# Kernel tuning notes

Hardware: AMD Instinct MI355X
Metric: run time of the kernel (lower is better)

## Reference

```python
import jax, jax.numpy as jnp
import numpy as np

NODES_PER_GRAPH = 57
NUM_BRANCHES = 80
NUM_GRAPHS = 4096
IN_CH = 4
HID = 128
NUM_LAYERS = 5
BN_EPS = 1e-5


def setup_inputs() -> dict:
    key = jax.random.key(0)
    ks = jax.random.split(key, 24)
    N = NUM_GRAPHS * NODES_PER_GRAPH
    E = NUM_GRAPHS * NUM_BRANCHES * 2  # bidirectional branches per graph
    x = jax.random.normal(ks[0], (N, IN_CH), dtype=jnp.float32)
    # within-graph random edges, offset per graph block
    ep = jax.random.randint(ks[1], (2, E), 0, NODES_PER_GRAPH, dtype=jnp.int32)
    off = jnp.repeat(jnp.arange(NUM_GRAPHS, dtype=jnp.int32) * NODES_PER_GRAPH,
                     NUM_BRANCHES * 2)
    edge_index = ep + off[None, :]
    i = np.arange(NUM_BRANCHES)
    branch_u = jnp.asarray(i % NODES_PER_GRAPH, dtype=jnp.int32)
    branch_v = jnp.asarray((i * 7 + 3) % NODES_PER_GRAPH, dtype=jnp.int32)
    s = 0.05
    return {
        "x": x, "edge_index": edge_index,
        "branch_u": branch_u, "branch_v": branch_v,
        "Wp": jax.random.normal(ks[2], (IN_CH, HID)) * s,
        "bp": jnp.zeros((HID,), jnp.float32),
        "conv_W": jax.random.normal(ks[3], (NUM_LAYERS, HID, HID)) * s,
        "conv_b": jnp.zeros((NUM_LAYERS, HID), jnp.float32),
        "bn_gamma": jnp.ones((NUM_LAYERS, HID), jnp.float32),
        "bn_beta": jnp.zeros((NUM_LAYERS, HID), jnp.float32),
        "bn_mean": jax.random.normal(ks[4], (NUM_LAYERS, HID)) * 0.1,
        "bn_var": jax.random.uniform(ks[5], (NUM_LAYERS, HID)) + 0.5,
        "phys_W1": jax.random.normal(ks[6], (HID, 16)) * s,
        "phys_b1": jnp.zeros((16,), jnp.float32),
        "phys_W2": jax.random.normal(ks[7], (16, 1)) * s,
        "phys_b2": jnp.zeros((1,), jnp.float32),
        "mlp_W1": jax.random.normal(ks[8], (2 * HID + 1, HID)) * s,
        "mlp_b1": jnp.zeros((HID,), jnp.float32),
        "mlp_W2": jax.random.normal(ks[9], (HID, 1)) * s,
        "mlp_b2": jnp.zeros((1,), jnp.float32),
    }


def _gcn_conv(x, edge_index, W, b, num_nodes):
    # PyG GCNConv: add self-loops, symmetric deg^{-1/2} normalization,
    # message = norm * (x @ W)[src], scatter-add into dst, then + bias.
    h = x @ W
    loop = jnp.arange(num_nodes, dtype=edge_index.dtype)
    src = jnp.concatenate([edge_index[0], loop])
    dst = jnp.concatenate([edge_index[1], loop])
    deg = jax.ops.segment_sum(jnp.ones_like(dst, dtype=h.dtype), dst,
                              num_segments=num_nodes)  # >= 1 (self-loop)
    dinv = jax.lax.rsqrt(deg)
    norm = dinv[src] * dinv[dst]  # [E+N]
    out = jax.ops.segment_sum(h[src] * norm[:, None], dst,
                              num_segments=num_nodes)
    return out + b


def _forward(x, edge_index, branch_u, branch_v, Wp, bp, conv_W, conv_b,
             bn_gamma, bn_beta, bn_mean, bn_var, phys_W1, phys_b1, phys_W2,
             phys_b2, mlp_W1, mlp_b1, mlp_W2, mlp_b2):
    N = x.shape[0]
    num_graphs = N // NODES_PER_GRAPH
    h = x @ Wp + bp
    for l in range(NUM_LAYERS):
        res = h
        h = _gcn_conv(h, edge_index, conv_W[l], conv_b[l], N)
        # BatchNorm1d in eval mode (running stats); dropout is identity in eval
        h = (h - bn_mean[l]) * jax.lax.rsqrt(bn_var[l] + BN_EPS) * bn_gamma[l] + bn_beta[l]
        h = jax.nn.relu(h)
        h = h + res
    theta = jax.nn.relu(h @ phys_W1 + phys_b1) @ phys_W2 + phys_b2  # [N,1]
    offsets = (jnp.arange(num_graphs, dtype=jnp.int32) * NODES_PER_GRAPH)
    u_idx = (branch_u[None, :] + offsets[:, None]).reshape(-1)
    v_idx = (branch_v[None, :] + offsets[:, None]).reshape(-1)
    edge_feat = jnp.concatenate([h[u_idx], h[v_idx]], axis=-1)  # [G*80, 2H]
    delta_theta = theta[u_idx] - theta[v_idx]                   # [G*80, 1]
    comb = jnp.concatenate([edge_feat, delta_theta], axis=-1)
    return jax.nn.relu(comb @ mlp_W1 + mlp_b1) @ mlp_W2 + mlp_b2


def reference(x, edge_index, branch_u, branch_v, Wp, bp, conv_W, conv_b,
              bn_gamma, bn_beta, bn_mean, bn_var, phys_W1, phys_b1, phys_W2,
              phys_b2, mlp_W1, mlp_b1, mlp_W2, mlp_b2):
    return _forward(x, edge_index, branch_u, branch_v, Wp, bp, conv_W, conv_b,
                    bn_gamma, bn_beta, bn_mean, bn_var, phys_W1, phys_b1,
                    phys_W2, phys_b2, mlp_W1, mlp_b1, mlp_W2, mlp_b2)
```

## Files before the change

### kernel.cpp

```cpp
#include <hip/hip_runtime.h>

#define NPG 57
#define NEPG 160
#define NB 80
#define HID 128
#define NG 4096
#define NL 5

typedef __attribute__((ext_vector_type(8))) short bf16x8;
typedef __attribute__((ext_vector_type(4))) float f32x4;
typedef unsigned int u32;

__device__ __forceinline__ short f2bf(float f) {
    u32 u = __builtin_bit_cast(u32, f);
    u += 0x7fff + ((u >> 16) & 1);
    return (short)(u >> 16);
}
__device__ __forceinline__ float bf2f(short s) {
    u32 u = ((u32)(unsigned short)s) << 16;
    return __builtin_bit_cast(float, u);
}
__device__ __forceinline__ u32 packhl(float v) {
    short hi = f2bf(v);
    short lo = f2bf(v - bf2f(hi));
    return (((u32)(unsigned short)hi) << 16) | (u32)(unsigned short)lo;
}
__device__ __forceinline__ float unpackf(u32 u) {
    return bf2f((short)(u >> 16)) + bf2f((short)(u & 0xFFFFu));
}

__device__ __forceinline__ void unpack_frag(uint4 a, uint4 b, bf16x8& fh, bf16x8& fl) {
    uint4 h, l;
    h.x = (a.y & 0xFFFF0000u) | (a.x >> 16);
    h.y = (a.w & 0xFFFF0000u) | (a.z >> 16);
    h.z = (b.y & 0xFFFF0000u) | (b.x >> 16);
    h.w = (b.w & 0xFFFF0000u) | (b.z >> 16);
    l.x = (a.y << 16) | (a.x & 0xFFFFu);
    l.y = (a.w << 16) | (a.z & 0xFFFFu);
    l.z = (b.y << 16) | (b.x & 0xFFFFu);
    l.w = (b.w << 16) | (b.z & 0xFFFFu);
    fh = __builtin_bit_cast(bf16x8, h);
    fl = __builtin_bit_cast(bf16x8, l);
}

__device__ __forceinline__ void frag_pk(const u32* rowp, int k0, int sw,
                                        bf16x8& fh, bf16x8& fl) {
    uint4 a = *(const uint4*)((const char*)rowp + ((k0 * 4) ^ sw));
    uint4 b = *(const uint4*)((const char*)rowp + (((k0 + 4) * 4) ^ sw));
    unpack_frag(a, b, fh, fl);
}

template<int NCT>
__device__ __forceinline__ void mm_ks(f32x4* acc, const bf16x8& fh, const bf16x8& fl,
                                      const short* __restrict__ whi,
                                      const short* __restrict__ wlo,
                                      int ln15, int kb, int ks, int ctbase) {
#pragma unroll
    for (int j = 0; j < NCT; ++j) {
        int ct = ctbase + j;
        bf16x8 bhi = *(const bf16x8*)(whi + (16 * ct + ln15) * HID + kb + 32 * ks);
        bf16x8 blo = *(const bf16x8*)(wlo + (16 * ct + ln15) * HID + kb + 32 * ks);
        f32x4 a = acc[j];
        a = __builtin_amdgcn_mfma_f32_16x16x32_bf16(fh, bhi, a, 0, 0, 0);
        a = __builtin_amdgcn_mfma_f32_16x16x32_bf16(fh, blo, a, 0, 0, 0);
        a = __builtin_amdgcn_mfma_f32_16x16x32_bf16(fl, bhi, a, 0, 0, 0);
        acc[j] = a;
    }
}

__global__ void prep(const float* __restrict__ convW, const float* __restrict__ mlpW1,
                     const float* __restrict__ physW1, const float* __restrict__ convb,
                     const float* __restrict__ bn_gamma, const float* __restrict__ bn_beta,
                     const float* __restrict__ bn_mean, const float* __restrict__ bn_var,
                     short* __restrict__ wb, float* __restrict__ fsc, float* __restrict__ fsh) {
    int id = blockIdx.x * 256 + threadIdx.x;
    if (id < 114688) {
        int mat = id >> 14, rem = id & 16383, n = rem >> 7, k = rem & 127;
        float w;
        if (mat < 5)       w = convW[mat * 16384 + k * 128 + n];
        else if (mat == 5) w = mlpW1[k * 128 + n];
        else               w = mlpW1[(128 + k) * 128 + n];
        short hi = f2bf(w);
        short lo = f2bf(w - bf2f(hi));
        wb[mat * 32768 + n * 128 + k] = hi;
        wb[mat * 32768 + 16384 + n * 128 + k] = lo;
    } else if (id < 116736) {
        int p = id - 114688, n = p >> 7, k = p & 127;
        float w = physW1[k * 16 + n];
        short hi = f2bf(w);
        short lo = f2bf(w - bf2f(hi));
        wb[229376 + p] = hi;
        wb[231424 + p] = lo;
    } else if (id < 117376) {
        int p = id - 116736;
        float sc = bn_gamma[p] * rsqrtf(bn_var[p] + 1e-5f);
        float sh = fmaf(convb[p] - bn_mean[p], sc, bn_beta[p]);
        fsc[p] = sc;
        fsh[p] = sh;
    }
}

__global__ __launch_bounds__(1024, 4) void pinn_fused(
    const float* __restrict__ x, const int* __restrict__ edge_index,
    const int* __restrict__ branch_u, const int* __restrict__ branch_v,
    const float* __restrict__ Wp, const float* __restrict__ bp,
    const float* __restrict__ physb1, const float* __restrict__ physW2,
    const float* __restrict__ physb2,
    const float* __restrict__ mlpW1, const float* __restrict__ mlpb1,
    const float* __restrict__ mlpW2, const float* __restrict__ mlpb2,
    const short* __restrict__ wb, const float* __restrict__ fsc,
    const float* __restrict__ fsh, float* __restrict__ out) {
    __shared__ u32  hTu[128][64];
    __shared__ u32  pool[64 * 128];
    __shared__ short Ahi[64 * 64];
    __shared__ short Alo[64 * 64];
    __shared__ float dinv[64];
    __shared__ int   deg[64];
    __shared__ short esrc[NEPG], edst[NEPG];
    __shared__ float theta[64];
    __shared__ float red[NB];
    __shared__ int   bu[NB], bv[NB];

    const int g = blockIdx.x;
    const int tid = threadIdx.x;
    const int lane = tid & 63;
    const int wv = tid >> 6;
    const int ln15 = lane & 15;
    const int hi4 = lane >> 4;
    const int kb = hi4 << 3;
    const int R0 = 16 * (wv & 3);
    const int ct0 = 2 * (wv >> 2);

    {
        int r = lane;
        float4 xv = make_float4(0.f, 0.f, 0.f, 0.f);
        if (r < NPG) xv = ((const float4*)x)[g * NPG + r];
        for (int c = 8 * wv; c < 8 * wv + 8; ++c) {
            float h0 = 0.f;
            if (r < NPG)
                h0 = fmaf(xv.x, Wp[c], fmaf(xv.y, Wp[HID + c],
                     fmaf(xv.z, Wp[2 * HID + c], fmaf(xv.w, Wp[3 * HID + c], bp[c]))));
            *(u32*)((char*)&hTu[c][0] + ((r * 4) ^ ((c & 7) << 4))) = packhl(h0);
        }
    }
    if (tid < 64) deg[tid] = (tid < NPG) ? 1 : 0;
    if (tid < NB) { bu[tid] = branch_u[tid]; bv[tid] = branch_v[tid]; red[tid] = 0.f; }
    {
        float* Af = (float*)pool;
        for (int i = tid; i < 4096; i += 1024) Af[i] = 0.f;
    }
    __syncthreads();

    if (tid < NEPG) {
        int gs = edge_index[g * NEPG + tid];
        int gd = edge_index[NG * NEPG + g * NEPG + tid];
        esrc[tid] = (short)(gs - g * NPG);
        edst[tid] = (short)(gd - g * NPG);
        atomicAdd(&deg[edst[tid]], 1);
    }
    __syncthreads();
    if (tid < 64) dinv[tid] = (tid < NPG) ? rsqrtf((float)deg[tid]) : 0.f;
    __syncthreads();
    {
        float* Af = (float*)pool;
        if (tid < NEPG) {
            int s = esrc[tid], d = edst[tid];
            atomicAdd(&Af[d * 64 + s], dinv[s] * dinv[d]);
        }
        if (tid < NPG) atomicAdd(&Af[tid * 64 + tid], dinv[tid] * dinv[tid]);
    }
    __syncthreads();
    {
        const float* Af = (const float*)pool;
        for (int i = tid; i < 4096; i += 1024) {
            float a = Af[i];
            short hi = f2bf(a);
            Ahi[i] = hi;
            Alo[i] = f2bf(a - bf2f(hi));
        }
    }
    __syncthreads();

    bf16x8 afh[2], afl[2];
#pragma unroll
    for (int ks2 = 0; ks2 < 2; ++ks2) {
        int off = (R0 + ln15) * 64 + 32 * ks2 + kb;
        afh[ks2] = *(const bf16x8*)&Ahi[off];
        afl[ks2] = *(const bf16x8*)&Alo[off];
    }

    u32* mpk = pool;
    for (int l = 0; l < NL; ++l) {
        f32x4 acc[2];
        acc[0] = (f32x4){0.f, 0.f, 0.f, 0.f};
        acc[1] = (f32x4){0.f, 0.f, 0.f, 0.f};
#pragma unroll
        for (int ks2 = 0; ks2 < 2; ++ks2) {
#pragma unroll
            for (int j = 0; j < 2; ++j) {
                int c = 16 * (ct0 + j) + ln15;
                bf16x8 hh, hl;
                frag_pk(&hTu[c][0], 32 * ks2 + kb, (c & 7) << 4, hh, hl);
                f32x4 a = acc[j];
                a = __builtin_amdgcn_mfma_f32_16x16x32_bf16(afh[ks2], hh, a, 0, 0, 0);
                a = __builtin_amdgcn_mfma_f32_16x16x32_bf16(afh[ks2], hl, a, 0, 0, 0);
                a = __builtin_amdgcn_mfma_f32_16x16x32_bf16(afl[ks2], hh, a, 0, 0, 0);
                acc[j] = a;
            }
        }
#pragma unroll
        for (int j = 0; j < 2; ++j) {
#pragma unroll
            for (int q = 0; q < 4; ++q) {
                int rr = R0 + 4 * hi4 + q;
                int cc = 16 * (ct0 + j) + ln15;
                *(u32*)((char*)&mpk[rr * 128] + ((cc * 4) ^ ((rr & 7) << 4))) =
                    packhl(acc[j][q]);
            }
        }
        __syncthreads();

        f32x4 z2[2];
        z2[0] = (f32x4){0.f, 0.f, 0.f, 0.f};
        z2[1] = (f32x4){0.f, 0.f, 0.f, 0.f};
        const short* whi = wb + 2 * l * 16384;
        const short* wlo = wb + (2 * l + 1) * 16384;
#pragma unroll
        for (int ks = 0; ks < 4; ++ks) {
            bf16x8 mh, ml;
            int rr = R0 + ln15;
            frag_pk(&mpk[rr * 128], 32 * ks + kb, (rr & 7) << 4, mh, ml);
            mm_ks<2>(z2, mh, ml, whi, wlo, ln15, kb, ks, ct0);
        }
        if (l == NL - 1) __syncthreads();

        const float* sc = fsc + l * HID;
        const float* sh = fsh + l * HID;
#pragma unroll
        for (int j = 0; j < 2; ++j) {
            int cc = 16 * (ct0 + j) + ln15;
            float scv = sc[cc], shv = sh[cc];
#pragma unroll
            for (int q = 0; q < 4; ++q) {
                int rr = R0 + 4 * hi4 + q;
                u32* hp = (u32*)((char*)&hTu[cc][0] + ((rr * 4) ^ ((cc & 7) << 4)));
                float hold = unpackf(*hp);
                float hnew = fmaxf(fmaf(z2[j][q], scv, shv), 0.f) + hold;
                if (l == NL - 1)
                    *(u32*)((char*)&pool[rr * 128] + ((cc * 4) ^ ((rr & 7) << 4))) =
                        packhl(hnew);
                else
                    *hp = packhl(hnew);
            }
        }
        __syncthreads();
    }

    if (wv < 4) {
        f32x4 t4 = (f32x4){0.f, 0.f, 0.f, 0.f};
        int r = 16 * wv + ln15;
#pragma unroll
        for (int ks = 0; ks < 4; ++ks) {
            bf16x8 fh, fl;
            frag_pk(&pool[r * 128], 32 * ks + kb, (r & 7) << 4, fh, fl);
            bf16x8 bh = *(const bf16x8*)(wb + 229376 + ln15 * HID + 32 * ks + kb);
            bf16x8 bl = *(const bf16x8*)(wb + 231424 + ln15 * HID + 32 * ks + kb);
            t4 = __builtin_amdgcn_mfma_f32_16x16x32_bf16(fh, bh, t4, 0, 0, 0);
            t4 = __builtin_amdgcn_mfma_f32_16x16x32_bf16(fh, bl, t4, 0, 0, 0);
            t4 = __builtin_amdgcn_mfma_f32_16x16x32_bf16(fl, bh, t4, 0, 0, 0);
        }
        float b1 = physb1[ln15], w2 = physW2[ln15], b2 = physb2[0];
#pragma unroll
        for (int q = 0; q < 4; ++q) {
            float val = fmaxf(t4[q] + b1, 0.f) * w2;
#pragma unroll
            for (int o = 1; o < 16; o <<= 1) val += __shfl_xor(val, o, 16);
            int rq = 16 * wv + 4 * hi4 + q;
            if (ln15 == 0 && rq < NPG) theta[rq] = val + b2;
        }
    }
    __syncthreads();

    for (int task = wv; task < 10; task += 16) {
        int t = task >> 1;
        int cb = (task & 1) * 4;
        int b = 16 * t + ln15;
        int ru = bu[b], rv = bv[b];
        f32x4 acc4[4];
#pragma unroll
        for (int j = 0; j < 4; ++j) acc4[j] = (f32x4){0.f, 0.f, 0.f, 0.f};
#pragma unroll
        for (int ks = 0; ks < 4; ++ks) {
            bf16x8 fh, fl;
            frag_pk(&pool[ru * 128], 32 * ks + kb, (ru & 7) << 4, fh, fl);
            mm_ks<4>(acc4, fh, fl, wb + 10 * 16384, wb + 11 * 16384, ln15, kb, ks, cb);
            frag_pk(&pool[rv * 128], 32 * ks + kb, (rv & 7) << 4, fh, fl);
            mm_ks<4>(acc4, fh, fl, wb + 12 * 16384, wb + 13 * 16384, ln15, kb, ks, cb);
        }
        float dth[4];
#pragma unroll
        for (int q = 0; q < 4; ++q) {
            int bb = 16 * t + 4 * hi4 + q;
            dth[q] = theta[bu[bb]] - theta[bv[bb]];
        }
        float sums[4] = {0.f, 0.f, 0.f, 0.f};
#pragma unroll
        for (int j = 0; j < 4; ++j) {
            int ch = 16 * (cb + j) + ln15;
            float w256 = mlpW1[256 * HID + ch];
            float b1 = mlpb1[ch];
            float w2 = mlpW2[ch];
#pragma unroll
            for (int q = 0; q < 4; ++q)
                sums[q] += fmaxf(fmaf(dth[q], w256, acc4[j][q] + b1), 0.f) * w2;
        }
#pragma unroll
        for (int q = 0; q < 4; ++q) {
#pragma unroll
            for (int o = 1; o < 16; o <<= 1) sums[q] += __shfl_xor(sums[q], o, 16);
            if (ln15 == 0) atomicAdd(&red[16 * t + 4 * hi4 + q], sums[q]);
        }
    }
    __syncthreads();
    if (tid < NB) out[g * NB + tid] = red[tid] + mlpb2[0];
}

extern "C" void kernel_launch(void* const* d_in, const int* in_sizes, int n_in,
                              void* d_out, int out_size, void* d_ws, size_t ws_size,
                              hipStream_t stream) {
    const float* x          = (const float*)d_in[0];
    const int*   edge_index = (const int*)d_in[1];
    const int*   branch_u   = (const int*)d_in[2];
    const int*   branch_v   = (const int*)d_in[3];
    const float* Wp         = (const float*)d_in[4];
    const float* bp         = (const float*)d_in[5];
    const float* convW      = (const float*)d_in[6];
    const float* convb      = (const float*)d_in[7];
    const float* bn_gamma   = (const float*)d_in[8];
    const float* bn_beta    = (const float*)d_in[9];
    const float* bn_mean    = (const float*)d_in[10];
    const float* bn_var     = (const float*)d_in[11];
    const float* physW1     = (const float*)d_in[12];
    const float* physb1     = (const float*)d_in[13];
    const float* physW2     = (const float*)d_in[14];
    const float* physb2     = (const float*)d_in[15];
    const float* mlpW1      = (const float*)d_in[16];
    const float* mlpb1      = (const float*)d_in[17];
    const float* mlpW2      = (const float*)d_in[18];
    const float* mlpb2      = (const float*)d_in[19];
    float* out = (float*)d_out;

    short* wb = (short*)d_ws;
    float* fsc = (float*)((char*)d_ws + 466944);
    float* fsh = fsc + 640;

    prep<<<459, 256, 0, stream>>>(convW, mlpW1, physW1, convb,
                                  bn_gamma, bn_beta, bn_mean, bn_var, wb, fsc, fsh);
    pinn_fused<<<NG, 1024, 0, stream>>>(
        x, edge_index, branch_u, branch_v, Wp, bp,
        physb1, physW2, physb2, mlpW1, mlpb1, mlpW2, mlpb2,
        wb, fsc, fsh, out);
}
```

Before: 1.221 ms.

## Switch split-precision MFMA from bf16 to fp16 with separate hi/lo planes, 512 threads

Replaces the bf16 hi/lo packed-u32 storage with separate fp16 hi and lo shared-memory planes and uses fp16 MFMA. This removes the per-fragment unpack bit manipulation and the pack/unpack work. The block shrinks from 1024 to 512 threads, so each wave now computes four column tiles instead of two. fp16 has a narrower exponent range than bf16, so the split may lose accuracy for very large or very small values, and fewer waves per block may reduce latency hiding.

```diff
diff --git a/kernel.cpp b/kernel.cpp
--- a/kernel.cpp
+++ b/kernel.cpp
@@ -7,72 +7,22 @@
 #define NG 4096
 #define NL 5
 
-typedef __attribute__((ext_vector_type(8))) short bf16x8;
+typedef __attribute__((ext_vector_type(8))) _Float16 f16x8;
+typedef __attribute__((ext_vector_type(4))) _Float16 f16x4;
 typedef __attribute__((ext_vector_type(4))) float f32x4;
-typedef unsigned int u32;
-
-__device__ __forceinline__ short f2bf(float f) {
-    u32 u = __builtin_bit_cast(u32, f);
-    u += 0x7fff + ((u >> 16) & 1);
-    return (short)(u >> 16);
-}
-__device__ __forceinline__ float bf2f(short s) {
-    u32 u = ((u32)(unsigned short)s) << 16;
-    return __builtin_bit_cast(float, u);
-}
-__device__ __forceinline__ u32 packhl(float v) {
-    short hi = f2bf(v);
-    short lo = f2bf(v - bf2f(hi));
-    return (((u32)(unsigned short)hi) << 16) | (u32)(unsigned short)lo;
-}
-__device__ __forceinline__ float unpackf(u32 u) {
-    return bf2f((short)(u >> 16)) + bf2f((short)(u & 0xFFFFu));
-}
-
-__device__ __forceinline__ void unpack_frag(uint4 a, uint4 b, bf16x8& fh, bf16x8& fl) {
-    uint4 h, l;
-    h.x = (a.y & 0xFFFF0000u) | (a.x >> 16);
-    h.y = (a.w & 0xFFFF0000u) | (a.z >> 16);
-    h.z = (b.y & 0xFFFF0000u) | (b.x >> 16);
-    h.w = (b.w & 0xFFFF0000u) | (b.z >> 16);
-    l.x = (a.y << 16) | (a.x & 0xFFFFu);
-    l.y = (a.w << 16) | (a.z & 0xFFFFu);
-    l.z = (b.y << 16) | (b.x & 0xFFFFu);
-    l.w = (b.w << 16) | (b.z & 0xFFFFu);
-    fh = __builtin_bit_cast(bf16x8, h);
-    fl = __builtin_bit_cast(bf16x8, l);
-}
-
-__device__ __forceinline__ void frag_pk(const u32* rowp, int k0, int sw,
-                                        bf16x8& fh, bf16x8& fl) {
-    uint4 a = *(const uint4*)((const char*)rowp + ((k0 * 4) ^ sw));
-    uint4 b = *(const uint4*)((const char*)rowp + (((k0 + 4) * 4) ^ sw));
-    unpack_frag(a, b, fh, fl);
-}
-
-template<int NCT>
-__device__ __forceinline__ void mm_ks(f32x4* acc, const bf16x8& fh, const bf16x8& fl,
-                                      const short* __restrict__ whi,
-                                      const short* __restrict__ wlo,
-                                      int ln15, int kb, int ks, int ctbase) {
-#pragma unroll
-    for (int j = 0; j < NCT; ++j) {
-        int ct = ctbase + j;
-        bf16x8 bhi = *(const bf16x8*)(whi + (16 * ct + ln15) * HID + kb + 32 * ks);
-        bf16x8 blo = *(const bf16x8*)(wlo + (16 * ct + ln15) * HID + kb + 32 * ks);
-        f32x4 a = acc[j];
-        a = __builtin_amdgcn_mfma_f32_16x16x32_bf16(fh, bhi, a, 0, 0, 0);
-        a = __builtin_amdgcn_mfma_f32_16x16x32_bf16(fh, blo, a, 0, 0, 0);
-        a = __builtin_amdgcn_mfma_f32_16x16x32_bf16(fl, bhi, a, 0, 0, 0);
-        acc[j] = a;
-    }
+
+#define MFMA16(A, B, C) __builtin_amdgcn_mfma_f32_16x16x32_f16(A, B, C, 0, 0, 0)
+
+__device__ __forceinline__ f16x8 ldf8(const _Float16* base, int byteoff) {
+    return *(const f16x8*)((const char*)base + byteoff);
 }
 
 __global__ void prep(const float* __restrict__ convW, const float* __restrict__ mlpW1,
                      const float* __restrict__ physW1, const float* __restrict__ convb,
                      const float* __restrict__ bn_gamma, const float* __restrict__ bn_beta,
                      const float* __restrict__ bn_mean, const float* __restrict__ bn_var,
-                     short* __restrict__ wb, float* __restrict__ fsc, float* __restrict__ fsh) {
+                     _Float16* __restrict__ wb, float* __restrict__ fsc,
+                     float* __restrict__ fsh) {
     int id = blockIdx.x * 256 + threadIdx.x;
     if (id < 114688) {
         int mat = id >> 14, rem = id & 16383, n = rem >> 7, k = rem & 127;
@@ -80,27 +30,24 @@
         if (mat < 5)       w = convW[mat * 16384 + k * 128 + n];
         else if (mat == 5) w = mlpW1[k * 128 + n];
         else               w = mlpW1[(128 + k) * 128 + n];
-        short hi = f2bf(w);
-        short lo = f2bf(w - bf2f(hi));
+        _Float16 hi = (_Float16)w;
         wb[mat * 32768 + n * 128 + k] = hi;
-        wb[mat * 32768 + 16384 + n * 128 + k] = lo;
+        wb[mat * 32768 + 16384 + n * 128 + k] = (_Float16)(w - (float)hi);
     } else if (id < 116736) {
         int p = id - 114688, n = p >> 7, k = p & 127;
         float w = physW1[k * 16 + n];
-        short hi = f2bf(w);
-        short lo = f2bf(w - bf2f(hi));
+        _Float16 hi = (_Float16)w;
         wb[229376 + p] = hi;
-        wb[231424 + p] = lo;
+        wb[231424 + p] = (_Float16)(w - (float)hi);
     } else if (id < 117376) {
         int p = id - 116736;
         float sc = bn_gamma[p] * rsqrtf(bn_var[p] + 1e-5f);
-        float sh = fmaf(convb[p] - bn_mean[p], sc, bn_beta[p]);
         fsc[p] = sc;
-        fsh[p] = sh;
+        fsh[p] = fmaf(convb[p] - bn_mean[p], sc, bn_beta[p]);
     }
 }
 
-__global__ __launch_bounds__(1024, 4) void pinn_fused(
+__global__ __launch_bounds__(512, 2) void pinn_fused(
     const float* __restrict__ x, const int* __restrict__ edge_index,
     const int* __restrict__ branch_u, const int* __restrict__ branch_v,
     const float* __restrict__ Wp, const float* __restrict__ bp,
@@ -108,12 +55,12 @@
     const float* __restrict__ physb2,
     const float* __restrict__ mlpW1, const float* __restrict__ mlpb1,
     const float* __restrict__ mlpW2, const float* __restrict__ mlpb2,
-    const short* __restrict__ wb, const float* __restrict__ fsc,
+    const _Float16* __restrict__ wb, const float* __restrict__ fsc,
     const float* __restrict__ fsh, float* __restrict__ out) {
-    __shared__ u32  hTu[128][64];
-    __shared__ u32  pool[64 * 128];
-    __shared__ short Ahi[64 * 64];
-    __shared__ short Alo[64 * 64];
+    __shared__ _Float16 hTh[128 * 64];
+    __shared__ _Float16 hTl[128 * 64];
+    __shared__ _Float16 mh[64 * 128];
+    __shared__ _Float16 ml[64 * 128];
     __shared__ float dinv[64];
     __shared__ int   deg[64];
     __shared__ short esrc[NEPG], edst[NEPG];
@@ -127,28 +74,32 @@
     const int wv = tid >> 6;
     const int ln15 = lane & 15;
     const int hi4 = lane >> 4;
-    const int kb = hi4 << 3;
     const int R0 = 16 * (wv & 3);
-    const int ct0 = 2 * (wv >> 2);
+    const int ct0 = 4 * (wv >> 2);
+
+    float* Af = (float*)mh;
+    _Float16* Ah = ml;
+    _Float16* Al = ml + 4096;
 
     {
-        int r = lane;
-        float4 xv = make_float4(0.f, 0.f, 0.f, 0.f);
-        if (r < NPG) xv = ((const float4*)x)[g * NPG + r];
-        for (int c = 8 * wv; c < 8 * wv + 8; ++c) {
+        int c = tid & 127;
+        int sw = (c & 7) << 4;
+        float w0 = Wp[c], w1 = Wp[HID + c], w2 = Wp[2 * HID + c], w3 = Wp[3 * HID + c];
+        float bb = bp[c];
+        for (int r = tid >> 7; r < 64; r += 4) {
             float h0 = 0.f;
-            if (r < NPG)
-                h0 = fmaf(xv.x, Wp[c], fmaf(xv.y, Wp[HID + c],
-                     fmaf(xv.z, Wp[2 * HID + c], fmaf(xv.w, Wp[3 * HID + c], bp[c]))));
-            *(u32*)((char*)&hTu[c][0] + ((r * 4) ^ ((c & 7) << 4))) = packhl(h0);
-        }
-    }
+            if (r < NPG) {
+                float4 xv = ((const float4*)x)[g * NPG + r];
+                h0 = fmaf(xv.x, w0, fmaf(xv.y, w1, fmaf(xv.z, w2, fmaf(xv.w, w3, bb))));
+            }
+            _Float16 hh = (_Float16)h0;
+            *(_Float16*)((char*)(hTh + c * 64) + ((r * 2) ^ sw)) = hh;
+            *(_Float16*)((char*)(hTl + c * 64) + ((r * 2) ^ sw)) = (_Float16)(h0 - (float)hh);
+        }
+    }
+    for (int i = tid; i < 4096; i += 512) Af[i] = 0.f;
     if (tid < 64) deg[tid] = (tid < NPG) ? 1 : 0;
     if (tid < NB) { bu[tid] = branch_u[tid]; bv[tid] = branch_v[tid]; red[tid] = 0.f; }
-    {
-        float* Af = (float*)pool;
-        for (int i = tid; i < 4096; i += 1024) Af[i] = 0.f;
-    }
     __syncthreads();
 
     if (tid < NEPG) {
@@ -161,113 +112,152 @@
     __syncthreads();
     if (tid < 64) dinv[tid] = (tid < NPG) ? rsqrtf((float)deg[tid]) : 0.f;
     __syncthreads();
+    if (tid < NEPG) {
+        int s = esrc[tid], d = edst[tid];
+        atomicAdd(&Af[d * 64 + s], dinv[s] * dinv[d]);
+    }
+    if (tid < NPG) atomicAdd(&Af[tid * 64 + tid], dinv[tid] * dinv[tid]);
+    __syncthreads();
+    for (int i = tid; i < 4096; i += 512) {
+        int r = i >> 6, s = i & 63;
+        float v = Af[i];
+        _Float16 hi = (_Float16)v;
+        int byteoff = (s * 2) ^ ((r & 7) << 4);
+        *(_Float16*)((char*)(Ah + r * 64) + byteoff) = hi;
+        *(_Float16*)((char*)(Al + r * 64) + byteoff) = (_Float16)(v - (float)hi);
+    }
+    __syncthreads();
+
+    f16x8 Ahf[2], Alf[2];
     {
-        float* Af = (float*)pool;
-        if (tid < NEPG) {
-            int s = esrc[tid], d = edst[tid];
-            atomicAdd(&Af[d * 64 + s], dinv[s] * dinv[d]);
-        }
-        if (tid < NPG) atomicAdd(&Af[tid * 64 + tid], dinv[tid] * dinv[tid]);
-    }
-    __syncthreads();
-    {
-        const float* Af = (const float*)pool;
-        for (int i = tid; i < 4096; i += 1024) {
-            float a = Af[i];
-            short hi = f2bf(a);
-            Ahi[i] = hi;
-            Alo[i] = f2bf(a - bf2f(hi));
-        }
-    }
-    __syncthreads();
-
-    bf16x8 afh[2], afl[2];
-#pragma unroll
-    for (int ks2 = 0; ks2 < 2; ++ks2) {
-        int off = (R0 + ln15) * 64 + 32 * ks2 + kb;
-        afh[ks2] = *(const bf16x8*)&Ahi[off];
-        afl[ks2] = *(const bf16x8*)&Alo[off];
-    }
-
-    u32* mpk = pool;
+        int ar = R0 + ln15;
+        int swr = (ar & 7) << 4;
+        Ahf[0] = ldf8(Ah + ar * 64, ((8 * hi4) * 2) ^ swr);
+        Ahf[1] = ldf8(Ah + ar * 64, ((32 + 8 * hi4) * 2) ^ swr);
+        Alf[0] = ldf8(Al + ar * 64, ((8 * hi4) * 2) ^ swr);
+        Alf[1] = ldf8(Al + ar * 64, ((32 + 8 * hi4) * 2) ^ swr);
+    }
+    __syncthreads();
+
+    const int mrow = R0 + ln15;
+    const int swm = (mrow & 7) << 4;
+
     for (int l = 0; l < NL; ++l) {
-        f32x4 acc[2];
-        acc[0] = (f32x4){0.f, 0.f, 0.f, 0.f};
-        acc[1] = (f32x4){0.f, 0.f, 0.f, 0.f};
+        f32x4 macc[4];
+#pragma unroll
+        for (int j = 0; j < 4; ++j) macc[j] = (f32x4){0.f, 0.f, 0.f, 0.f};
 #pragma unroll
         for (int ks2 = 0; ks2 < 2; ++ks2) {
 #pragma unroll
-            for (int j = 0; j < 2; ++j) {
+            for (int j = 0; j < 4; ++j) {
                 int c = 16 * (ct0 + j) + ln15;
-                bf16x8 hh, hl;
-                frag_pk(&hTu[c][0], 32 * ks2 + kb, (c & 7) << 4, hh, hl);
-                f32x4 a = acc[j];
-                a = __builtin_amdgcn_mfma_f32_16x16x32_bf16(afh[ks2], hh, a, 0, 0, 0);
-                a = __builtin_amdgcn_mfma_f32_16x16x32_bf16(afh[ks2], hl, a, 0, 0, 0);
-                a = __builtin_amdgcn_mfma_f32_16x16x32_bf16(afl[ks2], hh, a, 0, 0, 0);
-                acc[j] = a;
-            }
-        }
-#pragma unroll
-        for (int j = 0; j < 2; ++j) {
+                int byteoff = ((32 * ks2 + 8 * hi4) * 2) ^ ((c & 7) << 4);
+                f16x8 hh = ldf8(hTh + c * 64, byteoff);
+                f16x8 hl = ldf8(hTl + c * 64, byteoff);
+                f32x4 a = macc[j];
+                a = MFMA16(Ahf[ks2], hh, a);
+                a = MFMA16(Ahf[ks2], hl, a);
+                a = MFMA16(Alf[ks2], hh, a);
+                macc[j] = a;
+            }
+        }
+#pragma unroll
+        for (int j = 0; j < 4; ++j) {
+            int c = 16 * (ct0 + j) + ln15;
 #pragma unroll
             for (int q = 0; q < 4; ++q) {
-                int rr = R0 + 4 * hi4 + q;
-                int cc = 16 * (ct0 + j) + ln15;
-                *(u32*)((char*)&mpk[rr * 128] + ((cc * 4) ^ ((rr & 7) << 4))) =
-                    packhl(acc[j][q]);
+                int r = R0 + 4 * hi4 + q;
+                float v = macc[j][q];
+                _Float16 vh = (_Float16)v;
+                int byteoff = (c * 2) ^ ((r & 7) << 4);
+                *(_Float16*)((char*)(mh + r * 128) + byteoff) = vh;
+                *(_Float16*)((char*)(ml + r * 128) + byteoff) = (_Float16)(v - (float)vh);
             }
         }
         __syncthreads();
 
-        f32x4 z2[2];
-        z2[0] = (f32x4){0.f, 0.f, 0.f, 0.f};
-        z2[1] = (f32x4){0.f, 0.f, 0.f, 0.f};
-        const short* whi = wb + 2 * l * 16384;
-        const short* wlo = wb + (2 * l + 1) * 16384;
+        const _Float16* whi = wb + 2 * l * 16384;
+        const _Float16* wlo = wb + (2 * l + 1) * 16384;
+        f32x4 zacc[4];
+#pragma unroll
+        for (int j = 0; j < 4; ++j) zacc[j] = (f32x4){0.f, 0.f, 0.f, 0.f};
 #pragma unroll
         for (int ks = 0; ks < 4; ++ks) {
-            bf16x8 mh, ml;
-            int rr = R0 + ln15;
-            frag_pk(&mpk[rr * 128], 32 * ks + kb, (rr & 7) << 4, mh, ml);
-            mm_ks<2>(z2, mh, ml, whi, wlo, ln15, kb, ks, ct0);
-        }
-        if (l == NL - 1) __syncthreads();
-
-        const float* sc = fsc + l * HID;
-        const float* sh = fsh + l * HID;
-#pragma unroll
-        for (int j = 0; j < 2; ++j) {
-            int cc = 16 * (ct0 + j) + ln15;
-            float scv = sc[cc], shv = sh[cc];
-#pragma unroll
-            for (int q = 0; q < 4; ++q) {
-                int rr = R0 + 4 * hi4 + q;
-                u32* hp = (u32*)((char*)&hTu[cc][0] + ((rr * 4) ^ ((cc & 7) << 4)));
-                float hold = unpackf(*hp);
-                float hnew = fmaxf(fmaf(z2[j][q], scv, shv), 0.f) + hold;
-                if (l == NL - 1)
-                    *(u32*)((char*)&pool[rr * 128] + ((cc * 4) ^ ((rr & 7) << 4))) =
-                        packhl(hnew);
-                else
-                    *hp = packhl(hnew);
-            }
-        }
-        __syncthreads();
+            int byteoff = ((32 * ks + 8 * hi4) * 2) ^ swm;
+            f16x8 mhf = ldf8(mh + mrow * 128, byteoff);
+            f16x8 mlf = ldf8(ml + mrow * 128, byteoff);
+#pragma unroll
+            for (int j = 0; j < 4; ++j) {
+                int n = 16 * (ct0 + j) + ln15;
+                f16x8 bh = *(const f16x8*)(whi + n * 128 + 32 * ks + 8 * hi4);
+                f16x8 bl = *(const f16x8*)(wlo + n * 128 + 32 * ks + 8 * hi4);
+                f32x4 a = zacc[j];
+                a = MFMA16(mhf, bh, a);
+                a = MFMA16(mhf, bl, a);
+                a = MFMA16(mlf, bh, a);
+                zacc[j] = a;
+            }
+        }
+
+        if (l < NL - 1) {
+#pragma unroll
+            for (int j = 0; j < 4; ++j) {
+                int c = 16 * (ct0 + j) + ln15;
+                float scv = fsc[l * HID + c], shv = fsh[l * HID + c];
+                int byteoff = ((R0 + 4 * hi4) * 2) ^ ((c & 7) << 4);
+                f16x4 rh = *(const f16x4*)((const char*)(hTh + c * 64) + byteoff);
+                f16x4 rl = *(const f16x4*)((const char*)(hTl + c * 64) + byteoff);
+                f16x4 nh, nl;
+#pragma unroll
+                for (int q = 0; q < 4; ++q) {
+                    float hold = (float)rh[q] + (float)rl[q];
+                    float hnew = fmaxf(fmaf(zacc[j][q], scv, shv), 0.f) + hold;
+                    _Float16 vh = (_Float16)hnew;
+                    nh[q] = vh;
+                    nl[q] = (_Float16)(hnew - (float)vh);
+                }
+                *(f16x4*)((char*)(hTh + c * 64) + byteoff) = nh;
+                *(f16x4*)((char*)(hTl + c * 64) + byteoff) = nl;
+            }
+            __syncthreads();
+        } else {
+            __syncthreads();
+#pragma unroll
+            for (int j = 0; j < 4; ++j) {
+                int c = 16 * (ct0 + j) + ln15;
+                float scv = fsc[l * HID + c], shv = fsh[l * HID + c];
+                int tbyte = ((R0 + 4 * hi4) * 2) ^ ((c & 7) << 4);
+                f16x4 rh = *(const f16x4*)((const char*)(hTh + c * 64) + tbyte);
+                f16x4 rl = *(const f16x4*)((const char*)(hTl + c * 64) + tbyte);
+#pragma unroll
+                for (int q = 0; q < 4; ++q) {
+                    int r = R0 + 4 * hi4 + q;
+                    float hold = (float)rh[q] + (float)rl[q];
+                    float hnew = fmaxf(fmaf(zacc[j][q], scv, shv), 0.f) + hold;
+                    _Float16 vh = (_Float16)hnew;
+                    int byteoff = (c * 2) ^ ((r & 7) << 4);
+                    *(_Float16*)((char*)(mh + r * 128) + byteoff) = vh;
+                    *(_Float16*)((char*)(ml + r * 128) + byteoff) = (_Float16)(hnew - (float)vh);
+                }
+            }
+            __syncthreads();
+        }
     }
 
     if (wv < 4) {
         f32x4 t4 = (f32x4){0.f, 0.f, 0.f, 0.f};
         int r = 16 * wv + ln15;
+        int swr = (r & 7) << 4;
 #pragma unroll
         for (int ks = 0; ks < 4; ++ks) {
-            bf16x8 fh, fl;
-            frag_pk(&pool[r * 128], 32 * ks + kb, (r & 7) << 4, fh, fl);
-            bf16x8 bh = *(const bf16x8*)(wb + 229376 + ln15 * HID + 32 * ks + kb);
-            bf16x8 bl = *(const bf16x8*)(wb + 231424 + ln15 * HID + 32 * ks + kb);
-            t4 = __builtin_amdgcn_mfma_f32_16x16x32_bf16(fh, bh, t4, 0, 0, 0);
-            t4 = __builtin_amdgcn_mfma_f32_16x16x32_bf16(fh, bl, t4, 0, 0, 0);
-            t4 = __builtin_amdgcn_mfma_f32_16x16x32_bf16(fl, bh, t4, 0, 0, 0);
+            int byteoff = ((32 * ks + 8 * hi4) * 2) ^ swr;
+            f16x8 fh = ldf8(mh + r * 128, byteoff);
+            f16x8 fl = ldf8(ml + r * 128, byteoff);
+            f16x8 bh = *(const f16x8*)(wb + 229376 + ln15 * 128 + 32 * ks + 8 * hi4);
+            f16x8 bl = *(const f16x8*)(wb + 231424 + ln15 * 128 + 32 * ks + 8 * hi4);
+            t4 = MFMA16(fh, bh, t4);
+            t4 = MFMA16(fh, bl, t4);
+            t4 = MFMA16(fl, bh, t4);
         }
         float b1 = physb1[ln15], w2 = physW2[ln15], b2 = physb2[0];
 #pragma unroll
@@ -281,21 +271,47 @@
     }
     __syncthreads();
 
-    for (int task = wv; task < 10; task += 16) {
+    for (int task = wv; task < 10; task += 8) {
         int t = task >> 1;
-        int cb = (task & 1) * 4;
+        int cb = 4 * (task & 1);
         int b = 16 * t + ln15;
         int ru = bu[b], rv = bv[b];
         f32x4 acc4[4];
 #pragma unroll
         for (int j = 0; j < 4; ++j) acc4[j] = (f32x4){0.f, 0.f, 0.f, 0.f};
+        const _Float16* ph = wb + 10 * 16384;
+        const _Float16* pl = wb + 11 * 16384;
+        const _Float16* qh = wb + 12 * 16384;
+        const _Float16* ql = wb + 13 * 16384;
 #pragma unroll
         for (int ks = 0; ks < 4; ++ks) {
-            bf16x8 fh, fl;
-            frag_pk(&pool[ru * 128], 32 * ks + kb, (ru & 7) << 4, fh, fl);
-            mm_ks<4>(acc4, fh, fl, wb + 10 * 16384, wb + 11 * 16384, ln15, kb, ks, cb);
-            frag_pk(&pool[rv * 128], 32 * ks + kb, (rv & 7) << 4, fh, fl);
-            mm_ks<4>(acc4, fh, fl, wb + 12 * 16384, wb + 13 * 16384, ln15, kb, ks, cb);
+            int ko = 32 * ks + 8 * hi4;
+            f16x8 uh = ldf8(mh + ru * 128, ((ko * 2) ^ ((ru & 7) << 4)));
+            f16x8 ul = ldf8(ml + ru * 128, ((ko * 2) ^ ((ru & 7) << 4)));
+#pragma unroll
+            for (int j = 0; j < 4; ++j) {
+                int n = 16 * (cb + j) + ln15;
+                f16x8 bh = *(const f16x8*)(ph + n * 128 + ko);
+                f16x8 bl = *(const f16x8*)(pl + n * 128 + ko);
+                f32x4 a = acc4[j];
+                a = MFMA16(uh, bh, a);
+                a = MFMA16(uh, bl, a);
+                a = MFMA16(ul, bh, a);
+                acc4[j] = a;
+            }
+            f16x8 vh = ldf8(mh + rv * 128, ((ko * 2) ^ ((rv & 7) << 4)));
+            f16x8 vl = ldf8(ml + rv * 128, ((ko * 2) ^ ((rv & 7) << 4)));
+#pragma unroll
+            for (int j = 0; j < 4; ++j) {
+                int n = 16 * (cb + j) + ln15;
+                f16x8 bh = *(const f16x8*)(qh + n * 128 + ko);
+                f16x8 bl = *(const f16x8*)(ql + n * 128 + ko);
+                f32x4 a = acc4[j];
+                a = MFMA16(vh, bh, a);
+                a = MFMA16(vh, bl, a);
+                a = MFMA16(vl, bh, a);
+                acc4[j] = a;
+            }
         }
         float dth[4];
 #pragma unroll
@@ -350,13 +366,13 @@
     const float* mlpb2      = (const float*)d_in[19];
     float* out = (float*)d_out;
 
-    short* wb = (short*)d_ws;
+    _Float16* wb = (_Float16*)d_ws;
     float* fsc = (float*)((char*)d_ws + 466944);
     float* fsh = fsc + 640;
 
     prep<<<459, 256, 0, stream>>>(convW, mlpW1, physW1, convb,
                                   bn_gamma, bn_beta, bn_mean, bn_var, wb, fsc, fsh);
-    pinn_fused<<<NG, 1024, 0, stream>>>(
+    pinn_fused<<<NG, 512, 0, stream>>>(
         x, edge_index, branch_u, branch_v, Wp, bp,
         physb1, physW2, physb2, mlpW1, mlpb1, mlpW2, mlpb2,
         wb, fsc, fsh, out);
```

Measured after the change: 1.223 ms. About the same (+0.2%).
